# Optimization experiments

Hardware: AMD Instinct MI355X
Metric: run time of the kernel (lower is better)

Reference implementation:

```python
import jax, jax.numpy as jnp
import numpy as np

N_NODES = 50000
N_EDGES = 600000
D = 128
N_LAYERS = 4  # 2 base + 2 resnet layers
N_GRAPHS = 64
NEG_SLOPE = 0.01  # F.leaky_relu default


def setup_inputs() -> dict:
    key = jax.random.key(0)
    k1, k2, k3, k4, k5 = jax.random.split(key, 5)
    x = jax.random.normal(k1, (N_NODES, D), dtype=jnp.float32)
    edge_index = jax.random.randint(k2, (2, N_EDGES), 0, N_NODES, dtype=jnp.int64)
    batch = jnp.sort(jax.random.randint(k3, (N_NODES,), 0, N_GRAPHS, dtype=jnp.int64))
    Wl = jax.random.normal(k4, (N_LAYERS, D, D), dtype=jnp.float32) * 0.05
    bl = jnp.zeros((N_LAYERS, D), dtype=jnp.float32)
    Wr = jax.random.normal(k5, (N_LAYERS, D, D), dtype=jnp.float32) * 0.05
    return {"x": x, "edge_index": edge_index, "batch": batch,
            "Wl": Wl, "bl": bl, "Wr": Wr}


def _mean_aggregate(x, src, dst, n_nodes):
    # mean over incoming neighbors; isolated nodes get 0 (PyG scatter-mean semantics)
    s = jax.ops.segment_sum(x[src], dst, num_segments=n_nodes)  # [N, D]
    cnt = jax.ops.segment_sum(jnp.ones((src.shape[0],), x.dtype), dst,
                              num_segments=n_nodes)
    return s / jnp.maximum(cnt, 1.0)[:, None]


def reference(x, edge_index, batch, Wl, bl, Wr):
    src, dst = edge_index[0], edge_index[1]
    n = x.shape[0]
    for i in range(N_LAYERS):
        agg = _mean_aggregate(x, src, dst, n)                      # [N, D]
        # SAGEConv: lin_l(agg) + lin_r(x); lin_l has bias, lin_r does not
        x_new = agg @ Wl[i].T + bl[i] + x @ Wr[i].T
        x_new = jnp.where(x_new >= 0, x_new, NEG_SLOPE * x_new)    # leaky_relu
        x = x_new if i < 2 else x + x_new                          # residual after first 2
    # global mean pool per graph
    pooled = jax.ops.segment_sum(x, batch, num_segments=N_GRAPHS)  # [G, D]
    counts = jax.ops.segment_sum(jnp.ones((n,), x.dtype), batch,
                                 num_segments=N_GRAPHS)
    return pooled / jnp.maximum(counts, 1.0)[:, None]
```

## Files before the change

kernel.cpp:

```cpp
#include <hip/hip_runtime.h>

#define N_NODES 50000
#define N_EDGES 600000
#define DIM 128
#define N_LAYERS 4
#define N_GRAPHS 64
#define NEG_SLOPE 0.01f
#define NB_SCAN ((N_NODES + 255) / 256)
#define RS 264

typedef __attribute__((ext_vector_type(8))) short short8;
typedef __attribute__((ext_vector_type(16))) float floatx16;

__device__ __forceinline__ unsigned short f2bf(float f) {
    union { float f; unsigned u; } c; c.f = f;
    unsigned u = c.u;
    unsigned r = (u + 0x7FFFu + ((u >> 16) & 1u)) >> 16;
    return (unsigned short)r;
}
__device__ __forceinline__ float bfraw2f(unsigned short b) {
    union { unsigned u; float f; } c; c.u = ((unsigned)b) << 16;
    return c.f;
}
__device__ __forceinline__ float bflo(unsigned u) {
    union { unsigned u; float f; } c; c.u = u << 16; return c.f;
}
__device__ __forceinline__ float bfhi(unsigned u) {
    union { unsigned u; float f; } c; c.u = u & 0xFFFF0000u; return c.f;
}


__global__ void zero_ints(int* p, int n) {
    int i = blockIdx.x * blockDim.x + threadIdx.x;
    if (i < n) p[i] = 0;
}

__global__ void convert_x(const float4* __restrict__ x, uint4* __restrict__ xb) {
    int i = blockIdx.x * blockDim.x + threadIdx.x;
    if (i >= N_NODES * DIM / 8) return;
    float4 a = x[i * 2], b = x[i * 2 + 1];
    uint4 o;
    o.x = ((unsigned)f2bf(a.y) << 16) | f2bf(a.x);
    o.y = ((unsigned)f2bf(a.w) << 16) | f2bf(a.z);
    o.z = ((unsigned)f2bf(b.y) << 16) | f2bf(b.x);
    o.w = ((unsigned)f2bf(b.w) << 16) | f2bf(b.z);
    xb[i] = o;
}

__global__ void pack_w(const float* __restrict__ Wl, const float* __restrict__ Wr,
                       ushort* __restrict__ wpk) {
    int s = blockIdx.x >> 2, t = blockIdx.x & 3;
    int m = blockIdx.y, layer = blockIdx.z;
    int l = threadIdx.x;
    const float* W = ((m == 0) ? Wl : Wr) + (size_t)layer * DIM * DIM;
    int n = t * 32 + (l & 31);
    int kb = s * 16 + (l >> 5) * 8;
    size_t off = ((((size_t)(layer * 2 + m) * 8 + s) * 4 + t) * 64 + l) * 8;
    for (int j = 0; j < 8; j++)
        wpk[off + j] = f2bf(W[n * DIM + kb + j]);
}

__global__ void count_deg(const int* __restrict__ dst, int* deg) {
    int e = blockIdx.x * blockDim.x + threadIdx.x;
    if (e < N_EDGES) atomicAdd(&deg[dst[e]], 1);
}

__global__ void scan_pass1(const int* __restrict__ deg, int* __restrict__ bsum) {
    int i = blockIdx.x * 256 + threadIdx.x;
    int v = (i < N_NODES) ? deg[i] : 0;
    for (int off = 32; off > 0; off >>= 1) v += __shfl_down(v, off, 64);
    __shared__ int ws[4];
    int lane = threadIdx.x & 63, w = threadIdx.x >> 6;
    if (lane == 0) ws[w] = v;
    __syncthreads();
    if (threadIdx.x == 0) bsum[blockIdx.x] = ws[0] + ws[1] + ws[2] + ws[3];
}

__global__ void scan_pass2(int* __restrict__ bsum) {
    __shared__ int sm[256];
    int t = threadIdx.x;
    int v = (t < NB_SCAN) ? bsum[t] : 0;
    sm[t] = v;
    __syncthreads();
    for (int off = 1; off < 256; off <<= 1) {
        int u = (t >= off) ? sm[t - off] : 0;
        __syncthreads();
        sm[t] += u;
        __syncthreads();
    }
    if (t < NB_SCAN) bsum[t] = sm[t] - v;
}

__global__ void scan_pass3(const int* __restrict__ deg, const int* __restrict__ bsum,
                           int* __restrict__ rp) {
    int i = blockIdx.x * 256 + threadIdx.x;
    int v = (i < N_NODES) ? deg[i] : 0;
    int lane = threadIdx.x & 63, w = threadIdx.x >> 6;
    int s = v;
    for (int off = 1; off < 64; off <<= 1) {
        int t = __shfl_up(s, off, 64);
        if (lane >= off) s += t;
    }
    __shared__ int ws[4];
    if (lane == 63) ws[w] = s;
    __syncthreads();
    int wo = 0;
    for (int k = 0; k < 4; k++) wo += (k < w) ? ws[k] : 0;
    int incl = s + wo + bsum[blockIdx.x];
    if (i < N_NODES) rp[i + 1] = incl;
    if (i == 0) rp[0] = 0;
}

__global__ void fill_csr(const int* __restrict__ src, const int* __restrict__ dst,
                         const int* __restrict__ rp, int* __restrict__ fill,
                         int* __restrict__ csr) {
    int e = blockIdx.x * blockDim.x + threadIdx.x;
    if (e >= N_EDGES) return;
    int d = dst[e];
    int pos = atomicAdd(&fill[d], 1);
    csr[rp[d] + pos] = src[e];
}

__global__ void graph_start(const int* __restrict__ batch, int* __restrict__ gstart) {
    int i = blockIdx.x * blockDim.x + threadIdx.x;
    if (i >= N_NODES) return;
    int b = batch[i];
    if (i == 0) {
        for (int g = 0; g <= b; g++) gstart[g] = 0;
    } else {
        int p = batch[i - 1];
        for (int g = p + 1; g <= b; g++) gstart[g] = i;
    }
    if (i == N_NODES - 1) {
        for (int g = b + 1; g <= N_GRAPHS; g++) gstart[g] = N_NODES;
    }
}

__global__ __launch_bounds__(256) void agg_mean_wave4(const uint4* __restrict__ x16B,
                                                      const int* __restrict__ rp,
                                                      const int* __restrict__ csr,
                                                      uint4* __restrict__ agg16B) {
    int wv = threadIdx.x >> 6, lane = threadIdx.x & 63;
    int node = blockIdx.x * 4 + wv;
    if (node >= N_NODES) return;
    int s = rp[node], e = rp[node + 1];
    int ll = lane & 15, eg = lane >> 4;
    float a0 = 0.f, a1 = 0.f, a2 = 0.f, a3 = 0.f, a4 = 0.f, a5 = 0.f, a6 = 0.f, a7 = 0.f;
    for (int base = s; base < e; base += 64) {
        int cnt = min(64, e - base);
        unsigned myidx = (base + lane < e) ? (unsigned)csr[base + lane] : 0u;
        for (int j = 0; j < cnt; j += 16) {
            uint4 v[4];
#pragma unroll
            for (int k = 0; k < 4; k++) {
                int sel = j + k * 4 + eg;
                unsigned idx = __shfl(myidx, sel, 64);
                v[k] = make_uint4(0u, 0u, 0u, 0u);
                if (sel < cnt) v[k] = x16B[(size_t)idx * 16 + ll];
            }
#pragma unroll
            for (int k = 0; k < 4; k++) {
                a0 += bflo(v[k].x); a1 += bfhi(v[k].x);
                a2 += bflo(v[k].y); a3 += bfhi(v[k].y);
                a4 += bflo(v[k].z); a5 += bfhi(v[k].z);
                a6 += bflo(v[k].w); a7 += bfhi(v[k].w);
            }
        }
    }
    a0 += __shfl_xor(a0, 16, 64); a0 += __shfl_xor(a0, 32, 64);
    a1 += __shfl_xor(a1, 16, 64); a1 += __shfl_xor(a1, 32, 64);
    a2 += __shfl_xor(a2, 16, 64); a2 += __shfl_xor(a2, 32, 64);
    a3 += __shfl_xor(a3, 16, 64); a3 += __shfl_xor(a3, 32, 64);
    a4 += __shfl_xor(a4, 16, 64); a4 += __shfl_xor(a4, 32, 64);
    a5 += __shfl_xor(a5, 16, 64); a5 += __shfl_xor(a5, 32, 64);
    a6 += __shfl_xor(a6, 16, 64); a6 += __shfl_xor(a6, 32, 64);
    a7 += __shfl_xor(a7, 16, 64); a7 += __shfl_xor(a7, 32, 64);
    if (eg == 0) {
        float inv = 1.0f / (float)max(e - s, 1);
        uint4 o;
        o.x = ((unsigned)f2bf(a1 * inv) << 16) | f2bf(a0 * inv);
        o.y = ((unsigned)f2bf(a3 * inv) << 16) | f2bf(a2 * inv);
        o.z = ((unsigned)f2bf(a5 * inv) << 16) | f2bf(a4 * inv);
        o.w = ((unsigned)f2bf(a7 * inv) << 16) | f2bf(a6 * inv);
        agg16B[(size_t)node * 16 + ll] = o;
    }
}

__global__ __launch_bounds__(256) void fused_layer_mfma(const ushort* __restrict__ agg,
                                                        const ushort* __restrict__ xin,
                                                        ushort* __restrict__ xout,
                                                        const ushort* __restrict__ wpk,
                                                        const float* __restrict__ bias,
                                                        int residual) {
    __shared__ ushort sA[128 * RS];
    int t = threadIdx.x;
    int node0 = blockIdx.x * 128;

    const uint4* aggv = (const uint4*)(agg + (size_t)node0 * DIM);
    const uint4* xv   = (const uint4*)(xin + (size_t)node0 * DIM);
    for (int i = t; i < 128 * 32; i += 256) {
        int r = i >> 5, c = i & 31;
        uint4 val = make_uint4(0u, 0u, 0u, 0u);
        if (node0 + r < N_NODES)
            val = (c < 16) ? aggv[r * 16 + c] : xv[r * 16 + (c - 16)];
        *(uint4*)&sA[r * RS + c * 8] = val;
    }
    __syncthreads();

    int wv = t >> 6, l = t & 63;
    int m0 = wv * 32;
    const ushort* arow = &sA[(m0 + (l & 31)) * RS];
    int khalf = (l >> 5) * 8;

    floatx16 acc0, acc1, acc2, acc3;
    for (int ii = 0; ii < 16; ii++) acc0[ii] = acc1[ii] = acc2[ii] = acc3[ii] = 0.f;

    const ushort* wl8 = wpk + (size_t)l * 8;
#pragma unroll
    for (int s2 = 0; s2 < 16; s2++) {
        int m = s2 >> 3, s = s2 & 7;
        short8 a = *(const short8*)(arow + m * 128 + s * 16 + khalf);
        size_t fb = (size_t)((m * 8 + s) * 4) * 512;
        short8 b0 = *(const short8*)(wl8 + fb);
        short8 b1 = *(const short8*)(wl8 + fb + 512);
        short8 b2 = *(const short8*)(wl8 + fb + 1024);
        short8 b3 = *(const short8*)(wl8 + fb + 1536);
        acc0 = __builtin_amdgcn_mfma_f32_32x32x16_bf16(a, b0, acc0, 0, 0, 0);
        acc1 = __builtin_amdgcn_mfma_f32_32x32x16_bf16(a, b1, acc1, 0, 0, 0);
        acc2 = __builtin_amdgcn_mfma_f32_32x32x16_bf16(a, b2, acc2, 0, 0, 0);
        acc3 = __builtin_amdgcn_mfma_f32_32x32x16_bf16(a, b3, acc3, 0, 0, 0);
    }

    int col = l & 31;
    int rbase = 4 * (l >> 5);
    floatx16 accs[4] = {acc0, acc1, acc2, acc3};
    for (int t4 = 0; t4 < 4; t4++) {
        int n = t4 * 32 + col;
        float bv = bias[n];
#pragma unroll
        for (int r = 0; r < 16; r++) {
            int row = (r & 3) + 8 * (r >> 2) + rbase;
            int gm = m0 + row;
            int gn = node0 + gm;
            if (gn >= N_NODES) continue;
            float v = accs[t4][r] + bv;
            v = (v >= 0.f) ? v : NEG_SLOPE * v;
            if (residual) v += bfraw2f(sA[gm * RS + 128 + n]);
            xout[(size_t)gn * DIM + n] = f2bf(v);
        }
    }
}

__global__ __launch_bounds__(128) void pool_partial(const ushort* __restrict__ xb,
                                                    const int* __restrict__ batch,
                                                    float* __restrict__ pooled) {
    int nb = blockIdx.x * 128;
    int ne = min(nb + 128, N_NODES);
    int d = threadIdx.x;
    int gcur = batch[nb];
    float acc = 0.f;
    for (int n = nb; n < ne; n++) {
        int g = batch[n];
        if (g != gcur) {
            atomicAdd(&pooled[gcur * DIM + d], acc);
            acc = 0.f;
            gcur = g;
        }
        acc += bfraw2f(xb[(size_t)n * DIM + d]);
    }
    atomicAdd(&pooled[gcur * DIM + d], acc);
}

__global__ void pool_final(const float* __restrict__ pooled,
                           const int* __restrict__ gstart,
                           float* __restrict__ out) {
    int i = blockIdx.x * blockDim.x + threadIdx.x;
    if (i >= N_GRAPHS * DIM) return;
    int g = i >> 7;
    int cnt = gstart[g + 1] - gstart[g];
    out[i] = pooled[i] / (float)max(cnt, 1);
}


extern "C" void kernel_launch(void* const* d_in, const int* in_sizes, int n_in,
                              void* d_out, int out_size, void* d_ws, size_t ws_size,
                              hipStream_t stream) {
    const float* x     = (const float*)d_in[0];
    const int*   ei    = (const int*)d_in[1];
    const int*   batch = (const int*)d_in[2];
    const float* Wl    = (const float*)d_in[3];
    const float* bl    = (const float*)d_in[4];
    const float* Wr    = (const float*)d_in[5];
    float* out = (float*)d_out;

    const int* esrc = ei;
    const int* edst = ei + N_EDGES;

    ushort* xb0  = (ushort*)d_ws;
    ushort* xbuf = xb0 + (size_t)N_NODES * DIM;
    ushort* agg  = xbuf + (size_t)N_NODES * DIM;
    ushort* wpk  = agg + (size_t)N_NODES * DIM;
    int* deg    = (int*)(wpk + (size_t)N_LAYERS * 2 * DIM * DIM);
    int* fill   = deg + N_NODES;
    int* csr    = fill + N_NODES;
    int* rp     = csr + N_EDGES;
    int* gstart = rp + (N_NODES + 1);
    int* bsum   = gstart + (N_GRAPHS + 1);
    float* pooled = (float*)(bsum + NB_SCAN);

    zero_ints<<<(2 * N_NODES + 255) / 256, 256, 0, stream>>>(deg, 2 * N_NODES);
    zero_ints<<<(N_GRAPHS * DIM + 255) / 256, 256, 0, stream>>>((int*)pooled, N_GRAPHS * DIM);

    convert_x<<<(N_NODES * DIM / 8 + 255) / 256, 256, 0, stream>>>((const float4*)x, (uint4*)xb0);
    pack_w<<<dim3(32, 2, 4), 64, 0, stream>>>(Wl, Wr, wpk);
    count_deg<<<(N_EDGES + 255) / 256, 256, 0, stream>>>(edst, deg);

    scan_pass1<<<NB_SCAN, 256, 0, stream>>>(deg, bsum);
    scan_pass2<<<1, 256, 0, stream>>>(bsum);
    scan_pass3<<<NB_SCAN, 256, 0, stream>>>(deg, bsum, rp);

    fill_csr<<<(N_EDGES + 255) / 256, 256, 0, stream>>>(esrc, edst, rp, fill, csr);
    graph_start<<<(N_NODES + 255) / 256, 256, 0, stream>>>(batch, gstart);

    int agg_blocks = (N_NODES + 3) / 4;
    int gemm_blocks = (N_NODES + 127) / 128;
    for (int l = 0; l < N_LAYERS; l++) {
        const ushort* xin = (l == 0) ? xb0 : xbuf;
        agg_mean_wave4<<<agg_blocks, 256, 0, stream>>>((const uint4*)xin, rp, csr, (uint4*)agg);
        fused_layer_mfma<<<gemm_blocks, 256, 0, stream>>>(
            agg, xin, xbuf, wpk + (size_t)l * 2 * DIM * DIM,
            bl + (size_t)l * DIM, (l >= 2) ? 1 : 0);
    }

    pool_partial<<<(N_NODES + 127) / 128, 128, 0, stream>>>(xbuf, batch, pooled);
    pool_final<<<(N_GRAPHS * DIM + 255) / 256, 256, 0, stream>>>(pooled, gstart, out);
}
```

Baseline: 367.5 us.

## Merge preprocessing launches and shrink GEMM tile to 64 rows

Folds the zeroing, x conversion, weight packing and degree counting into fewer launches, and merges CSR fill with graph-start computation. This cuts per-launch overhead in the setup phase. It also halves the fused layer GEMM block to 64 nodes, with each wave computing two 32-column tiles, and adds launch bounds for 4 blocks per CU. The smaller tile is meant to raise occupancy and block count over the 50k rows, at the cost of reloading weights more often.

```diff
diff --git a/kernel.cpp b/kernel.cpp
--- a/kernel.cpp
+++ b/kernel.cpp
@@ -7,6 +7,9 @@
 #define N_GRAPHS 64
 #define NEG_SLOPE 0.01f
 #define NB_SCAN ((N_NODES + 255) / 256)
+#define NB_CNT ((N_EDGES + 255) / 256)
+#define NC_CONV (N_NODES * DIM / 8 / 256)
+#define NB_PACK 64
 #define RS 264
 
 typedef __attribute__((ext_vector_type(8))) short short8;
@@ -29,40 +32,40 @@
     union { unsigned u; float f; } c; c.u = u & 0xFFFF0000u; return c.f;
 }
 
-
-__global__ void zero_ints(int* p, int n) {
+__global__ void zero2(int* a, int na, int* b, int nb) {
     int i = blockIdx.x * blockDim.x + threadIdx.x;
-    if (i < n) p[i] = 0;
-}
-
-__global__ void convert_x(const float4* __restrict__ x, uint4* __restrict__ xb) {
-    int i = blockIdx.x * blockDim.x + threadIdx.x;
-    if (i >= N_NODES * DIM / 8) return;
-    float4 a = x[i * 2], b = x[i * 2 + 1];
-    uint4 o;
-    o.x = ((unsigned)f2bf(a.y) << 16) | f2bf(a.x);
-    o.y = ((unsigned)f2bf(a.w) << 16) | f2bf(a.z);
-    o.z = ((unsigned)f2bf(b.y) << 16) | f2bf(b.x);
-    o.w = ((unsigned)f2bf(b.w) << 16) | f2bf(b.z);
-    xb[i] = o;
-}
-
-__global__ void pack_w(const float* __restrict__ Wl, const float* __restrict__ Wr,
-                       ushort* __restrict__ wpk) {
-    int s = blockIdx.x >> 2, t = blockIdx.x & 3;
-    int m = blockIdx.y, layer = blockIdx.z;
-    int l = threadIdx.x;
-    const float* W = ((m == 0) ? Wl : Wr) + (size_t)layer * DIM * DIM;
-    int n = t * 32 + (l & 31);
-    int kb = s * 16 + (l >> 5) * 8;
-    size_t off = ((((size_t)(layer * 2 + m) * 8 + s) * 4 + t) * 64 + l) * 8;
-    for (int j = 0; j < 8; j++)
-        wpk[off + j] = f2bf(W[n * DIM + kb + j]);
-}
-
-__global__ void count_deg(const int* __restrict__ dst, int* deg) {
-    int e = blockIdx.x * blockDim.x + threadIdx.x;
-    if (e < N_EDGES) atomicAdd(&deg[dst[e]], 1);
+    if (i < na) a[i] = 0;
+    else if (i < na + nb) b[i - na] = 0;
+}
+
+__global__ void preprocess(const float4* __restrict__ x, uint4* __restrict__ xb,
+                           const float* __restrict__ Wl, const float* __restrict__ Wr,
+                           ushort* __restrict__ wpk,
+                           const int* __restrict__ edst, int* __restrict__ deg) {
+    int b = blockIdx.x;
+    if (b < NC_CONV) {
+        int i = b * 256 + threadIdx.x;
+        float4 a = x[i * 2], c = x[i * 2 + 1];
+        uint4 o;
+        o.x = ((unsigned)f2bf(a.y) << 16) | f2bf(a.x);
+        o.y = ((unsigned)f2bf(a.w) << 16) | f2bf(a.z);
+        o.z = ((unsigned)f2bf(c.y) << 16) | f2bf(c.x);
+        o.w = ((unsigned)f2bf(c.w) << 16) | f2bf(c.z);
+        xb[i] = o;
+    } else if (b < NC_CONV + NB_PACK) {
+        int u = (b - NC_CONV) * 4 + (threadIdx.x >> 6);
+        int l = threadIdx.x & 63;
+        int layer = u >> 6, m = (u >> 5) & 1, s = (u >> 2) & 7, tt = u & 3;
+        const float* W = ((m == 0) ? Wl : Wr) + (size_t)layer * DIM * DIM;
+        int n = tt * 32 + (l & 31);
+        int kb = s * 16 + (l >> 5) * 8;
+        size_t off = ((size_t)u * 64 + l) * 8;
+        for (int j = 0; j < 8; j++)
+            wpk[off + j] = f2bf(W[n * DIM + kb + j]);
+    } else {
+        int e = (b - NC_CONV - NB_PACK) * 256 + threadIdx.x;
+        if (e < N_EDGES) atomicAdd(&deg[edst[e]], 1);
+    }
 }
 
 __global__ void scan_pass1(const int* __restrict__ deg, int* __restrict__ bsum) {
@@ -111,28 +114,30 @@
     if (i == 0) rp[0] = 0;
 }
 
-__global__ void fill_csr(const int* __restrict__ src, const int* __restrict__ dst,
-                         const int* __restrict__ rp, int* __restrict__ fill,
-                         int* __restrict__ csr) {
-    int e = blockIdx.x * blockDim.x + threadIdx.x;
-    if (e >= N_EDGES) return;
-    int d = dst[e];
-    int pos = atomicAdd(&fill[d], 1);
-    csr[rp[d] + pos] = src[e];
-}
-
-__global__ void graph_start(const int* __restrict__ batch, int* __restrict__ gstart) {
-    int i = blockIdx.x * blockDim.x + threadIdx.x;
-    if (i >= N_NODES) return;
-    int b = batch[i];
-    if (i == 0) {
-        for (int g = 0; g <= b; g++) gstart[g] = 0;
+__global__ void fill_gstart(const int* __restrict__ src, const int* __restrict__ dst,
+                            const int* __restrict__ rp, int* __restrict__ fill,
+                            int* __restrict__ csr,
+                            const int* __restrict__ batch, int* __restrict__ gstart) {
+    int b = blockIdx.x;
+    if (b < NB_CNT) {
+        int e = b * 256 + threadIdx.x;
+        if (e >= N_EDGES) return;
+        int d = dst[e];
+        int pos = atomicAdd(&fill[d], 1);
+        csr[rp[d] + pos] = src[e];
     } else {
-        int p = batch[i - 1];
-        for (int g = p + 1; g <= b; g++) gstart[g] = i;
-    }
-    if (i == N_NODES - 1) {
-        for (int g = b + 1; g <= N_GRAPHS; g++) gstart[g] = N_NODES;
+        int i = (b - NB_CNT) * 256 + threadIdx.x;
+        if (i >= N_NODES) return;
+        int g0 = batch[i];
+        if (i == 0) {
+            for (int g = 0; g <= g0; g++) gstart[g] = 0;
+        } else {
+            int p = batch[i - 1];
+            for (int g = p + 1; g <= g0; g++) gstart[g] = i;
+        }
+        if (i == N_NODES - 1) {
+            for (int g = g0 + 1; g <= N_GRAPHS; g++) gstart[g] = N_NODES;
+        }
     }
 }
 
@@ -186,19 +191,19 @@
     }
 }
 
-__global__ __launch_bounds__(256) void fused_layer_mfma(const ushort* __restrict__ agg,
-                                                        const ushort* __restrict__ xin,
-                                                        ushort* __restrict__ xout,
-                                                        const ushort* __restrict__ wpk,
-                                                        const float* __restrict__ bias,
-                                                        int residual) {
-    __shared__ ushort sA[128 * RS];
+__global__ __launch_bounds__(256, 4) void fused_layer_mfma(const ushort* __restrict__ agg,
+                                                           const ushort* __restrict__ xin,
+                                                           ushort* __restrict__ xout,
+                                                           const ushort* __restrict__ wpk,
+                                                           const float* __restrict__ bias,
+                                                           int residual) {
+    __shared__ ushort sA[64 * RS];
     int t = threadIdx.x;
-    int node0 = blockIdx.x * 128;
+    int node0 = blockIdx.x * 64;
 
     const uint4* aggv = (const uint4*)(agg + (size_t)node0 * DIM);
     const uint4* xv   = (const uint4*)(xin + (size_t)node0 * DIM);
-    for (int i = t; i < 128 * 32; i += 256) {
+    for (int i = t; i < 64 * 32; i += 256) {
         int r = i >> 5, c = i & 31;
         uint4 val = make_uint4(0u, 0u, 0u, 0u);
         if (node0 + r < N_NODES)
@@ -207,15 +212,16 @@
     }
     __syncthreads();
 
-    int wv = t >> 6, l = t & 63;
-    int m0 = wv * 32;
+    int w = t >> 6, l = t & 63;
+    int m0 = (w >> 1) * 32;
+    int th = w & 1;
     const ushort* arow = &sA[(m0 + (l & 31)) * RS];
     int khalf = (l >> 5) * 8;
 
-    floatx16 acc0, acc1, acc2, acc3;
-    for (int ii = 0; ii < 16; ii++) acc0[ii] = acc1[ii] = acc2[ii] = acc3[ii] = 0.f;
-
-    const ushort* wl8 = wpk + (size_t)l * 8;
+    floatx16 acc0, acc1;
+    for (int ii = 0; ii < 16; ii++) acc0[ii] = acc1[ii] = 0.f;
+
+    const ushort* wl8 = wpk + (size_t)l * 8 + (size_t)(2 * th) * 512;
 #pragma unroll
     for (int s2 = 0; s2 < 16; s2++) {
         int m = s2 >> 3, s = s2 & 7;
@@ -223,19 +229,15 @@
         size_t fb = (size_t)((m * 8 + s) * 4) * 512;
         short8 b0 = *(const short8*)(wl8 + fb);
         short8 b1 = *(const short8*)(wl8 + fb + 512);
-        short8 b2 = *(const short8*)(wl8 + fb + 1024);
-        short8 b3 = *(const short8*)(wl8 + fb + 1536);
         acc0 = __builtin_amdgcn_mfma_f32_32x32x16_bf16(a, b0, acc0, 0, 0, 0);
         acc1 = __builtin_amdgcn_mfma_f32_32x32x16_bf16(a, b1, acc1, 0, 0, 0);
-        acc2 = __builtin_amdgcn_mfma_f32_32x32x16_bf16(a, b2, acc2, 0, 0, 0);
-        acc3 = __builtin_amdgcn_mfma_f32_32x32x16_bf16(a, b3, acc3, 0, 0, 0);
     }
 
     int col = l & 31;
     int rbase = 4 * (l >> 5);
-    floatx16 accs[4] = {acc0, acc1, acc2, acc3};
-    for (int t4 = 0; t4 < 4; t4++) {
-        int n = t4 * 32 + col;
+    floatx16 accs[2] = {acc0, acc1};
+    for (int ti = 0; ti < 2; ti++) {
+        int n = (2 * th + ti) * 32 + col;
         float bv = bias[n];
 #pragma unroll
         for (int r = 0; r < 16; r++) {
@@ -243,7 +245,7 @@
             int gm = m0 + row;
             int gn = node0 + gm;
             if (gn >= N_NODES) continue;
-            float v = accs[t4][r] + bv;
+            float v = accs[ti][r] + bv;
             v = (v >= 0.f) ? v : NEG_SLOPE * v;
             if (residual) v += bfraw2f(sA[gm * RS + 128 + n]);
             xout[(size_t)gn * DIM + n] = f2bf(v);
@@ -308,22 +310,21 @@
     int* bsum   = gstart + (N_GRAPHS + 1);
     float* pooled = (float*)(bsum + NB_SCAN);
 
-    zero_ints<<<(2 * N_NODES + 255) / 256, 256, 0, stream>>>(deg, 2 * N_NODES);
-    zero_ints<<<(N_GRAPHS * DIM + 255) / 256, 256, 0, stream>>>((int*)pooled, N_GRAPHS * DIM);
-
-    convert_x<<<(N_NODES * DIM / 8 + 255) / 256, 256, 0, stream>>>((const float4*)x, (uint4*)xb0);
-    pack_w<<<dim3(32, 2, 4), 64, 0, stream>>>(Wl, Wr, wpk);
-    count_deg<<<(N_EDGES + 255) / 256, 256, 0, stream>>>(edst, deg);
+    zero2<<<(2 * N_NODES + N_GRAPHS * DIM + 255) / 256, 256, 0, stream>>>(
+        deg, 2 * N_NODES, (int*)pooled, N_GRAPHS * DIM);
+
+    preprocess<<<NC_CONV + NB_PACK + NB_CNT, 256, 0, stream>>>(
+        (const float4*)x, (uint4*)xb0, Wl, Wr, wpk, edst, deg);
 
     scan_pass1<<<NB_SCAN, 256, 0, stream>>>(deg, bsum);
     scan_pass2<<<1, 256, 0, stream>>>(bsum);
     scan_pass3<<<NB_SCAN, 256, 0, stream>>>(deg, bsum, rp);
 
-    fill_csr<<<(N_EDGES + 255) / 256, 256, 0, stream>>>(esrc, edst, rp, fill, csr);
-    graph_start<<<(N_NODES + 255) / 256, 256, 0, stream>>>(batch, gstart);
+    fill_gstart<<<NB_CNT + NB_SCAN, 256, 0, stream>>>(esrc, edst, rp, fill, csr,
+                                                      batch, gstart);
 
     int agg_blocks = (N_NODES + 3) / 4;
-    int gemm_blocks = (N_NODES + 127) / 128;
+    int gemm_blocks = (N_NODES + 63) / 64;
     for (int l = 0; l < N_LAYERS; l++) {
         const ushort* xin = (l == 0) ? xb0 : xbuf;
         agg_mean_wave4<<<agg_blocks, 256, 0, stream>>>((const uint4*)xin, rp, csr, (uint4*)agg);
```

Measured after the change: 337.0 us (median of 2 runs). 1.09x faster.
